# Performance work log

Hardware: AMD Instinct MI355X
Metric: run time of the kernel (lower is better)

## Reference

```python
import jax, jax.numpy as jnp
import numpy as np

MASS = 1.5
DT = 0.01      # physics.refresh_rate
EPS = 1e-6
B, STATE, ACT, T, H = 2048, 12, 4, 128, 512

_NORM = np.zeros(STATE, dtype=np.float32)
_NORM[0] = 4.0 / np.pi; _NORM[1] = 0.5; _NORM[2] = 4.0 / np.pi
_NORM[3] = 0.1; _NORM[4] = 1.0 / 60.0; _NORM[5] = 1.0 / 60.0
_NORM = jnp.asarray(_NORM)  # indices 6:12 stay zero (predict only normalizes 0:6)


def _leaky(x):
    return jnp.where(x >= 0, x, 0.01 * x)


def _mlp(x, W0, b0, W1, b1, W2, b2, W3, b3):
    # 3 hidden LeakyReLU layers + linear head (dropout is eval-mode identity)
    h = _leaky(x @ W0 + b0)
    h = _leaky(h @ W1 + b1)
    h = _leaky(h @ W2 + b2)
    return h @ W3 + b3


def _L_EB(phi, theta, psi):
    cph, sph = jnp.cos(phi), jnp.sin(phi)
    cth, sth = jnp.cos(theta), jnp.sin(theta)
    cps, sps = jnp.cos(psi), jnp.sin(psi)
    r1 = jnp.stack([cth * cps, sph * sth * cps - cph * sps, cph * sth * cps + sph * sps], -1)
    r2 = jnp.stack([cth * sps, sph * sth * sps + cph * cps, cph * sth * sps - sph * cps], -1)
    r3 = jnp.stack([-sth, sph * cth, cph * cth], -1)
    return jnp.stack([r1, r2, r3], -2)  # [B,3,3]


def _derivs(x, forces, I_mat, I_inv):
    V = x[:, 3:6]
    phi, theta = x[:, 6], x[:, 7]
    psi = x[:, 8]
    omega = x[:, 9:12]
    Fv, M = forces[:, 0:3], forces[:, 3:6]
    dpos = jnp.einsum('bij,bj->bi', _L_EB(phi, theta, psi), V)
    dvel = Fv / MASS - jnp.cross(omega, V)
    tth = jnp.tan(theta)
    cth = jnp.clip(jnp.cos(theta), EPS)
    sph, cph = jnp.sin(phi), jnp.cos(phi)
    one, zero = jnp.ones_like(phi), jnp.zeros_like(phi)
    J = jnp.stack([
        jnp.stack([one, sph * tth, cph * tth], -1),
        jnp.stack([zero, cph, -sph], -1),
        jnp.stack([zero, sph / cth, cph / cth], -1)], -2)  # [B,3,3]
    datt = jnp.einsum('bij,bj->bi', J, omega)
    Iw = omega @ I_mat.T                       # I @ omega
    coriolis = jnp.cross(omega, Iw)
    domega = (M - coriolis) @ I_inv.T
    return jnp.concatenate([dpos, dvel, datt, domega], axis=1)


def _rk4(x, forces, I_mat, I_inv):
    f = lambda s: _derivs(s, forces, I_mat, I_inv)
    k1 = f(x)
    k2 = f(x + 0.5 * DT * k1)
    k3 = f(x + 0.5 * DT * k2)
    k4 = f(x + DT * k3)
    return x + (DT / 6.0) * (k1 + 2 * k2 + 2 * k3 + k4)


def _predict(x, act, W, I_mat, I_inv):
    norm_x = x * _NORM
    norm_act = (act - 1500.0) / 500.0
    fn = _mlp(jnp.concatenate([norm_x, norm_act], axis=1), *W)
    zeros = jnp.zeros_like(fn[:, 0])
    forces = jnp.stack([fn[:, 0] - 0.5,
                        fn[:, 1] * -0.4 - 10.0,
                        fn[:, 2] * 0.2 - 0.1,
                        zeros, zeros, zeros], axis=1)
    return forces, _rk4(x, forces, I_mat, I_inv)


def setup_inputs() -> dict:
    key = jax.random.key(0)
    ks = jax.random.split(key, 12)
    x_t = jax.random.normal(ks[0], (B, STATE), dtype=jnp.float32) * 0.1
    act_inps = jax.random.uniform(ks[1], (B, ACT, T), dtype=jnp.float32,
                                  minval=1000.0, maxval=2000.0)
    I_mat = jnp.asarray([[0.02, 0.001, 0.002],
                         [0.001, 0.03, 0.001],
                         [0.002, 0.001, 0.04]], dtype=jnp.float32)
    def lin(k, fi, fo):
        s = np.sqrt(2.0 / (fi + fo)).astype(np.float32)
        return jax.random.normal(k, (fi, fo), dtype=jnp.float32) * s
    dims = [(STATE + ACT, H), (H, H), (H, H), (H, 6)]
    W = {}
    for i, (fi, fo) in enumerate(dims):
        W[f'W{i}'] = lin(ks[2 + i], fi, fo)
        W[f'b{i}'] = jnp.zeros((fo,), dtype=jnp.float32)
    return dict(x_t=x_t, act_inps=act_inps, I_mat=I_mat, seq_len=T, **W)


def reference(x_t, act_inps, I_mat, W0, b0, W1, b1, W2, b2, W3, b3, seq_len):
    I_inv = jnp.linalg.inv(I_mat)
    W = (W0, b0, W1, b1, W2, b2, W3, b3)
    acts = jnp.transpose(act_inps[:, :, 1:seq_len], (2, 0, 1))  # [T-1,B,ACT]

    def step(x, act):
        forces, nx = _predict(x, act, W, I_mat, I_inv)
        return nx, (forces, nx)

    _, (forces_seq, x_seq) = jax.lax.scan(step, x_t, acts)
    stacked = jnp.concatenate([x_t[:, :, None], jnp.transpose(x_seq, (1, 2, 0))], axis=2)  # [B,12,T]
    stackedForces = jnp.transpose(forces_seq, (1, 2, 0))  # [B,6,T-1]
    return stackedForces, stacked
```

## Files before the change

### kernel.cpp

```cpp
#include <hip/hip_runtime.h>
#include <stdint.h>

typedef unsigned short u16;
typedef unsigned int   u32;
typedef __attribute__((ext_vector_type(8))) short short8;
typedef __attribute__((ext_vector_type(4))) float f32x4;

#define B_TOT   2048
#define HID     512
#define T_FULL  128
#define ROWS    32
#define NWG     (B_TOT / ROWS)
#define THREADS 512
#define NT      4

#define W0F_SZ  16384
#define W1F_SZ  262144
#define W3F_SZ  8192
#define WF_TOTAL (W0F_SZ + 2*W1F_SZ + W3F_SZ)

__device__ __forceinline__ u16 f2bf(float f){
  u32 u = __float_as_uint(f);
  u32 r = (u + 0x7FFFu + ((u >> 16) & 1u)) >> 16;
  return (u16)r;
}

__device__ __forceinline__ int lds_idx(int m, int k){
  int chunk = k >> 3;
  return m * 512 + ((chunk ^ (m & 7)) << 3) + (k & 7);
}

__global__ void wm_repack(const float* __restrict__ W0, const float* __restrict__ W1,
                          const float* __restrict__ W2, const float* __restrict__ W3,
                          u16* __restrict__ wf)
{
  int idx = blockIdx.x * blockDim.x + threadIdx.x;
  if (idx >= WF_TOTAL) return;
  int e = idx;
  if (e < W0F_SZ){
    int j = e & 7, l = (e >> 3) & 63, nt = e >> 9;
    int k = ((l >> 4) << 3) + j, n = (nt << 4) + (l & 15);
    wf[idx] = (k < 16) ? f2bf(W0[k * HID + n]) : (u16)0;
    return;
  }
  e -= W0F_SZ;
  if (e < W1F_SZ){
    int j = e & 7, l = (e >> 3) & 63, rest = e >> 9, kt = rest & 15, nt = rest >> 4;
    int k = (kt << 5) + ((l >> 4) << 3) + j, n = (nt << 4) + (l & 15);
    wf[idx] = f2bf(W1[k * HID + n]);
    return;
  }
  e -= W1F_SZ;
  if (e < W1F_SZ){
    int j = e & 7, l = (e >> 3) & 63, rest = e >> 9, kt = rest & 15, nt = rest >> 4;
    int k = (kt << 5) + ((l >> 4) << 3) + j, n = (nt << 4) + (l & 15);
    wf[idx] = f2bf(W2[k * HID + n]);
    return;
  }
  e -= W1F_SZ;
  {
    int j = e & 7, l = (e >> 3) & 63, kt = e >> 9;
    int k = (kt << 5) + ((l >> 4) << 3) + j, n = l & 15;
    wf[idx] = (n < 6) ? f2bf(W3[k * 6 + n]) : (u16)0;
  }
}

__device__ __forceinline__ void invert3(const float* a, float* inv){
  float d = a[0]*(a[4]*a[8]-a[5]*a[7]) - a[1]*(a[3]*a[8]-a[5]*a[6]) + a[2]*(a[3]*a[7]-a[4]*a[6]);
  float id = 1.0f / d;
  inv[0]=(a[4]*a[8]-a[5]*a[7])*id; inv[1]=(a[2]*a[7]-a[1]*a[8])*id; inv[2]=(a[1]*a[5]-a[2]*a[4])*id;
  inv[3]=(a[5]*a[6]-a[3]*a[8])*id; inv[4]=(a[0]*a[8]-a[2]*a[6])*id; inv[5]=(a[2]*a[3]-a[0]*a[5])*id;
  inv[6]=(a[3]*a[7]-a[4]*a[6])*id; inv[7]=(a[1]*a[6]-a[0]*a[7])*id; inv[8]=(a[0]*a[4]-a[1]*a[3])*id;
}

__device__ __forceinline__ void derivs(const float* x, const float* Fv,
                                       const float* I9, const float* Ii, float* dx)
{
  float V0=x[3], V1=x[4], V2=x[5];
  float phi=x[6], th=x[7], psi=x[8];
  float w0=x[9], w1=x[10], w2=x[11];
  float sph=__sinf(phi), cph=__cosf(phi);
  float sth=__sinf(th),  cth=__cosf(th);
  float sps=__sinf(psi), cps=__cosf(psi);
  float r00=cth*cps, r01=sph*sth*cps - cph*sps, r02=cph*sth*cps + sph*sps;
  float r10=cth*sps, r11=sph*sth*sps + cph*cps, r12=cph*sth*sps - sph*cps;
  float r20=-sth,    r21=sph*cth,               r22=cph*cth;
  dx[0]=r00*V0+r01*V1+r02*V2;
  dx[1]=r10*V0+r11*V1+r12*V2;
  dx[2]=r20*V0+r21*V1+r22*V2;
  const float invm = 1.0f/1.5f;
  dx[3]=Fv[0]*invm - (w1*V2 - w2*V1);
  dx[4]=Fv[1]*invm - (w2*V0 - w0*V2);
  dx[5]=Fv[2]*invm - (w0*V1 - w1*V0);
  float tth = sth / cth;
  float rc  = 1.0f / fmaxf(cth, 1e-6f);
  dx[6]= w0 + sph*tth*w1 + cph*tth*w2;
  dx[7]=      cph*w1     - sph*w2;
  dx[8]=      sph*rc*w1  + cph*rc*w2;
  float Iw0=I9[0]*w0+I9[1]*w1+I9[2]*w2;
  float Iw1=I9[3]*w0+I9[4]*w1+I9[5]*w2;
  float Iw2=I9[6]*w0+I9[7]*w1+I9[8]*w2;
  float c0=w1*Iw2-w2*Iw1, c1=w2*Iw0-w0*Iw2, c2=w0*Iw1-w1*Iw0;
  dx[9] = -(Ii[0]*c0+Ii[1]*c1+Ii[2]*c2);
  dx[10]= -(Ii[3]*c0+Ii[4]*c1+Ii[5]*c2);
  dx[11]= -(Ii[6]*c0+Ii[7]*c1+Ii[8]*c2);
}

__device__ __forceinline__ void rk4(float* X, const float* Fv, const float* I9, const float* Ii){
  float k1[12],k2[12],k3[12],k4[12],xt[12];
  derivs(X,Fv,I9,Ii,k1);
  #pragma unroll
  for (int c=0;c<12;++c) xt[c]=X[c]+0.005f*k1[c];
  derivs(xt,Fv,I9,Ii,k2);
  #pragma unroll
  for (int c=0;c<12;++c) xt[c]=X[c]+0.005f*k2[c];
  derivs(xt,Fv,I9,Ii,k3);
  #pragma unroll
  for (int c=0;c<12;++c) xt[c]=X[c]+0.01f*k3[c];
  derivs(xt,Fv,I9,Ii,k4);
  #pragma unroll
  for (int c=0;c<12;++c) X[c]+=(0.01f/6.0f)*(k1[c]+2.0f*k2[c]+2.0f*k3[c]+k4[c]);
}

__device__ __forceinline__ void build_input(u16* bufA, const float* X,
                                            const float* __restrict__ act,
                                            int b, int r, int t)
{
  float vin[16];
  vin[0]=X[0]*1.2732395447351628f;
  vin[1]=X[1]*0.5f;
  vin[2]=X[2]*1.2732395447351628f;
  vin[3]=X[3]*0.1f;
  vin[4]=X[4]*0.016666666666666666f;
  vin[5]=X[5]*0.016666666666666666f;
  #pragma unroll
  for (int c=6;c<12;++c) vin[c]=0.0f;
  #pragma unroll
  for (int a=0;a<4;++a)
    vin[12+a] = (act[(size_t)(b*4+a)*T_FULL + t] - 1500.0f) * 0.002f;
  #pragma unroll
  for (int p=0;p<16;++p){
    u32 pack = 0u;
    if (p < 8) pack = (u32)f2bf(vin[2*p]) | ((u32)f2bf(vin[2*p+1]) << 16);
    ((u32*)bufA)[lds_idx(r, 2*p) >> 1] = pack;
  }
}

template<int KT>
__device__ __forceinline__ void do_layer(const u16* __restrict__ bufIn,
                                         const u16* __restrict__ wfrag,
                                         const float* __restrict__ bias,
                                         u16* __restrict__ bufOut,
                                         int lane, int ntb)
{
  const int lm = lane & 15, half = lane >> 4;
  const int m0 = lm, m1 = 16 + lm;
  const int sw0 = m0 & 7, sw1 = m1 & 7;
  f32x4 acc0[NT], acc1[NT];
  #pragma unroll
  for (int i=0;i<NT;++i){ acc0[i]=(f32x4)0.0f; acc1[i]=(f32x4)0.0f; }

  const u16* wbase = wfrag + (((size_t)ntb*KT*64 + lane) << 3);

  short8 Bf[2][NT];
  short8 A0[2], A1[2];
  {
    const int cb = half;
    A0[0] = *(const short8*)(bufIn + m0*512 + ((cb ^ sw0) << 3));
    A1[0] = *(const short8*)(bufIn + m1*512 + ((cb ^ sw1) << 3));
    #pragma unroll
    for (int i=0;i<NT;++i)
      Bf[0][i] = *(const short8*)(wbase + ((size_t)(i*KT) << 9));
  }
  #pragma unroll
  for (int kt=0; kt<KT; ++kt){
    const int cur = kt & 1, nxt = cur ^ 1;
    if (kt + 1 < KT){
      const int cb = ((kt+1) << 2) + half;
      A0[nxt] = *(const short8*)(bufIn + m0*512 + ((cb ^ sw0) << 3));
      A1[nxt] = *(const short8*)(bufIn + m1*512 + ((cb ^ sw1) << 3));
      #pragma unroll
      for (int i=0;i<NT;++i)
        Bf[nxt][i] = *(const short8*)(wbase + ((size_t)(i*KT + kt + 1) << 9));
    }
    #pragma unroll
    for (int i=0;i<NT;++i){
      acc0[i] = __builtin_amdgcn_mfma_f32_16x16x32_bf16(A0[cur], Bf[cur][i], acc0[i], 0, 0, 0);
      acc1[i] = __builtin_amdgcn_mfma_f32_16x16x32_bf16(A1[cur], Bf[cur][i], acc1[i], 0, 0, 0);
    }
  }
  #pragma unroll
  for (int i=0;i<NT;++i){
    int n = ((ntb + i) << 4) + lm;
    float bv = bias[n];
    #pragma unroll
    for (int reg=0; reg<4; ++reg){
      int r0 = (half << 2) + reg, r1 = 16 + r0;
      float v0 = acc0[i][reg] + bv; v0 = (v0 >= 0.0f) ? v0 : 0.01f*v0;
      float v1 = acc1[i][reg] + bv; v1 = (v1 >= 0.0f) ? v1 : 0.01f*v1;
      bufOut[lds_idx(r0, n)] = f2bf(v0);
      bufOut[lds_idx(r1, n)] = f2bf(v1);
    }
  }
}

__global__ __launch_bounds__(THREADS, 2)
void wm_main(const float* __restrict__ x_t, const float* __restrict__ act,
             const float* __restrict__ Imat, const int* __restrict__ seqlen_p,
             const float* __restrict__ b0, const float* __restrict__ b1,
             const float* __restrict__ b2, const float* __restrict__ b3,
             const u16* __restrict__ wf, float* __restrict__ out)
{
  __shared__ u16 bufA[16384];
  __shared__ u16 bufB[16384];
  float* fscr = (float*)(bufA + 256);
  const int tid  = threadIdx.x;
  const int lane = tid & 63;
  const int wave = tid >> 6;
  const int ntb  = wave * NT;
  const int rowbase = blockIdx.x * ROWS;
  const int steps = seqlen_p[0] - 1;
  const int seqlen = steps + 1;

  const u16* w0f = wf;
  const u16* w1f = wf + W0F_SZ;
  const u16* w2f = w1f + W1F_SZ;
  const u16* w3f = w2f + W1F_SZ;

  float* outF = out;
  float* outX = out + (size_t)B_TOT * 6 * steps;

  float X[12], I9[9], Ii[9];
  if (tid < ROWS){
    const int b = rowbase + tid;
    #pragma unroll
    for (int c=0;c<12;++c){
      float raw = x_t[b*12 + c];
      X[c] = raw;
      outX[(size_t)(b*12 + c)*seqlen] = raw;
    }
    #pragma unroll
    for (int i=0;i<9;++i) I9[i] = Imat[i];
    invert3(I9, Ii);
    build_input(bufA, X, act, b, tid, 1);
  }

  for (int s=0; s<steps; ++s){
    __syncthreads();
    do_layer<1 >(bufA, w0f, b0, bufB, lane, ntb);
    __syncthreads();
    do_layer<16>(bufB, w1f, b1, bufA, lane, ntb);
    __syncthreads();
    do_layer<16>(bufA, w2f, b2, bufB, lane, ntb);
    __syncthreads();
    if (wave == 0){
      const int lm = lane & 15, half = lane >> 4;
      const int m0 = lm, m1 = 16 + lm;
      const int sw0 = m0 & 7, sw1 = m1 & 7;
      short8 w3r[16];
      #pragma unroll
      for (int kt=0; kt<16; ++kt)
        w3r[kt] = *(const short8*)(w3f + (((size_t)kt*64 + lane) << 3));
      f32x4 a3_0 = (f32x4)0.0f, a3_1 = (f32x4)0.0f;
      #pragma unroll
      for (int kt=0; kt<16; ++kt){
        int cb = (kt << 2) + half;
        short8 x0 = *(const short8*)(bufB + m0*512 + ((cb ^ sw0) << 3));
        short8 x1 = *(const short8*)(bufB + m1*512 + ((cb ^ sw1) << 3));
        a3_0 = __builtin_amdgcn_mfma_f32_16x16x32_bf16(x0, w3r[kt], a3_0, 0, 0, 0);
        a3_1 = __builtin_amdgcn_mfma_f32_16x16x32_bf16(x1, w3r[kt], a3_1, 0, 0, 0);
      }
      const int c = lm;
      float bv = (c < 6) ? b3[c] : 0.0f;
      #pragma unroll
      for (int mt=0; mt<2; ++mt){
        #pragma unroll
        for (int reg=0; reg<4; ++reg){
          int rr = (mt << 4) + (half << 2) + reg;
          float fn = ((mt == 0) ? a3_0[reg] : a3_1[reg]) + bv;
          float f;
          if      (c == 0) f = fn - 0.5f;
          else if (c == 1) f = fn * -0.4f - 10.0f;
          else if (c == 2) f = fn * 0.2f - 0.1f;
          else             f = 0.0f;
          if (c < 6){
            int b = rowbase + rr;
            outF[(size_t)(b*6 + c)*steps + s] = f;
          }
          if (c < 3) fscr[rr*3 + c] = f;
        }
      }
      asm volatile("s_waitcnt lgkmcnt(0)" ::: "memory");
      if (tid < ROWS){
        const int b = rowbase + tid;
        float Fv[3] = { fscr[tid*3], fscr[tid*3+1], fscr[tid*3+2] };
        rk4(X, Fv, I9, Ii);
        #pragma unroll
        for (int cc=0;cc<12;++cc)
          outX[(size_t)(b*12 + cc)*seqlen + (s+1)] = X[cc];
        if (s + 1 < steps) build_input(bufA, X, act, b, tid, s + 2);
      }
    }
  }
}

extern "C" void kernel_launch(void* const* d_in, const int* in_sizes, int n_in,
                              void* d_out, int out_size, void* d_ws, size_t ws_size,
                              hipStream_t stream)
{
  const float* x_t  = (const float*)d_in[0];
  const float* act  = (const float*)d_in[1];
  const float* Imat = (const float*)d_in[2];
  const int*   seqp = (const int*)d_in[3];
  const float* W0   = (const float*)d_in[4];
  const float* b0   = (const float*)d_in[5];
  const float* W1   = (const float*)d_in[6];
  const float* b1   = (const float*)d_in[7];
  const float* W2   = (const float*)d_in[8];
  const float* b2   = (const float*)d_in[9];
  const float* W3   = (const float*)d_in[10];
  const float* b3   = (const float*)d_in[11];
  u16* wfrag = (u16*)d_ws;

  hipLaunchKernelGGL(wm_repack, dim3((WF_TOTAL + 255)/256), dim3(256), 0, stream,
                     W0, W1, W2, W3, wfrag);
  hipLaunchKernelGGL(wm_main, dim3(NWG), dim3(THREADS), 0, stream,
                     x_t, act, Imat, seqp, b0, b1, b2, b3, wfrag, (float*)d_out);
}
```

Measured before the change: 6.109 ms.

## Deepen weight prefetch to 4-k-tile blocks and recompute inertia inverse per step

The hidden-layer GEMM now loads weight fragments in blocks of four k-tiles with double buffering, and batches the LDS activation loads per block, where before it prefetched a single k-tile ahead. The aim is to keep more global weight loads in flight and hide their latency behind the MFMA work. The inertia matrix inverse is no longer kept in registers for the whole kernel; it is reloaded and inverted inside each step, which lowers register pressure at the cost of a little redundant scalar work. The larger Bf buffer (32 short8 values) raises VGPR use and may spill or reduce occupancy.

```diff
diff --git a/kernel.cpp b/kernel.cpp
--- a/kernel.cpp
+++ b/kernel.cpp
@@ -162,31 +162,50 @@
 
   const u16* wbase = wfrag + (((size_t)ntb*KT*64 + lane) << 3);
 
-  short8 Bf[2][NT];
-  short8 A0[2], A1[2];
-  {
-    const int cb = half;
-    A0[0] = *(const short8*)(bufIn + m0*512 + ((cb ^ sw0) << 3));
-    A1[0] = *(const short8*)(bufIn + m1*512 + ((cb ^ sw1) << 3));
+  if constexpr (KT == 1){
+    short8 A0 = *(const short8*)(bufIn + m0*512 + ((half ^ sw0) << 3));
+    short8 A1 = *(const short8*)(bufIn + m1*512 + ((half ^ sw1) << 3));
+    short8 Bf[NT];
     #pragma unroll
     for (int i=0;i<NT;++i)
-      Bf[0][i] = *(const short8*)(wbase + ((size_t)(i*KT) << 9));
-  }
-  #pragma unroll
-  for (int kt=0; kt<KT; ++kt){
-    const int cur = kt & 1, nxt = cur ^ 1;
-    if (kt + 1 < KT){
-      const int cb = ((kt+1) << 2) + half;
-      A0[nxt] = *(const short8*)(bufIn + m0*512 + ((cb ^ sw0) << 3));
-      A1[nxt] = *(const short8*)(bufIn + m1*512 + ((cb ^ sw1) << 3));
+      Bf[i] = *(const short8*)(wbase + ((size_t)i << 9));
+    #pragma unroll
+    for (int i=0;i<NT;++i){
+      acc0[i] = __builtin_amdgcn_mfma_f32_16x16x32_bf16(A0, Bf[i], acc0[i], 0, 0, 0);
+      acc1[i] = __builtin_amdgcn_mfma_f32_16x16x32_bf16(A1, Bf[i], acc1[i], 0, 0, 0);
+    }
+  } else {
+    static_assert(KT == 16, "KT must be 1 or 16");
+    short8 Bf[2][4][NT];
+    #pragma unroll
+    for (int j=0;j<4;++j)
       #pragma unroll
       for (int i=0;i<NT;++i)
-        Bf[nxt][i] = *(const short8*)(wbase + ((size_t)(i*KT + kt + 1) << 9));
-    }
-    #pragma unroll
-    for (int i=0;i<NT;++i){
-      acc0[i] = __builtin_amdgcn_mfma_f32_16x16x32_bf16(A0[cur], Bf[cur][i], acc0[i], 0, 0, 0);
-      acc1[i] = __builtin_amdgcn_mfma_f32_16x16x32_bf16(A1[cur], Bf[cur][i], acc1[i], 0, 0, 0);
+        Bf[0][j][i] = *(const short8*)(wbase + ((size_t)(i*KT + j) << 9));
+    #pragma unroll
+    for (int blk=0; blk<4; ++blk){
+      const int cur = blk & 1, nxt = cur ^ 1;
+      if (blk < 3){
+        #pragma unroll
+        for (int j=0;j<4;++j)
+          #pragma unroll
+          for (int i=0;i<NT;++i)
+            Bf[nxt][j][i] = *(const short8*)(wbase + ((size_t)(i*KT + blk*4 + 4 + j) << 9));
+      }
+      short8 A0[4], A1[4];
+      #pragma unroll
+      for (int j=0;j<4;++j){
+        const int cb = ((blk*4 + j) << 2) + half;
+        A0[j] = *(const short8*)(bufIn + m0*512 + ((cb ^ sw0) << 3));
+        A1[j] = *(const short8*)(bufIn + m1*512 + ((cb ^ sw1) << 3));
+      }
+      #pragma unroll
+      for (int j=0;j<4;++j)
+        #pragma unroll
+        for (int i=0;i<NT;++i){
+          acc0[i] = __builtin_amdgcn_mfma_f32_16x16x32_bf16(A0[j], Bf[cur][j][i], acc0[i], 0, 0, 0);
+          acc1[i] = __builtin_amdgcn_mfma_f32_16x16x32_bf16(A1[j], Bf[cur][j][i], acc1[i], 0, 0, 0);
+        }
     }
   }
   #pragma unroll
@@ -230,7 +249,7 @@
   float* outF = out;
   float* outX = out + (size_t)B_TOT * 6 * steps;
 
-  float X[12], I9[9], Ii[9];
+  float X[12];
   if (tid < ROWS){
     const int b = rowbase + tid;
     #pragma unroll
@@ -239,9 +258,6 @@
       X[c] = raw;
       outX[(size_t)(b*12 + c)*seqlen] = raw;
     }
-    #pragma unroll
-    for (int i=0;i<9;++i) I9[i] = Imat[i];
-    invert3(I9, Ii);
     build_input(bufA, X, act, b, tid, 1);
   }
 
@@ -293,6 +309,10 @@
       asm volatile("s_waitcnt lgkmcnt(0)" ::: "memory");
       if (tid < ROWS){
         const int b = rowbase + tid;
+        float I9[9], Ii[9];
+        #pragma unroll
+        for (int i=0;i<9;++i) I9[i] = Imat[i];
+        invert3(I9, Ii);
         float Fv[3] = { fscr[tid*3], fscr[tid*3+1], fscr[tid*3+2] };
         rk4(X, Fv, I9, Ii);
         #pragma unroll
```

New measurement: 5.598 ms. -8.4%, faster.

## Split hidden layers across four cooperating workgroups with global-memory exchange and flags

Applied to the files above, without the earlier changes.

Each 32-row batch group now runs on four workgroups. Each workgroup computes a quarter of the output columns of the two 512x512 hidden layers, then exchanges its slices with the other three through global memory, using per-layer flag counters and spin-waits. Layer 0 weights and the biases are held in registers, and only the first member writes outputs. This gives four times more parallel work per time step, so more CUs are busy, at the cost of two inter-workgroup synchronisations per step through global memory. It also depends on all 256 workgroups being resident at once to avoid deadlock.

```diff
diff --git a/kernel.cpp b/kernel.cpp
--- a/kernel.cpp
+++ b/kernel.cpp
@@ -10,14 +10,16 @@
 #define HID     512
 #define T_FULL  128
 #define ROWS    32
-#define NWG     (B_TOT / ROWS)
+#define NGRP    64
+#define NWG     256
 #define THREADS 512
-#define NT      4
+#define NMEM    4
 
 #define W0F_SZ  16384
 #define W1F_SZ  262144
 #define W3F_SZ  8192
 #define WF_TOTAL (W0F_SZ + 2*W1F_SZ + W3F_SZ)
+#define NFLAGS  (NGRP * 2 * NMEM)
 
 __device__ __forceinline__ u16 f2bf(float f){
   u32 u = __float_as_uint(f);
@@ -35,7 +37,11 @@
                           u16* __restrict__ wf)
 {
   int idx = blockIdx.x * blockDim.x + threadIdx.x;
-  if (idx >= WF_TOTAL) return;
+  if (idx >= WF_TOTAL){
+    int fi = idx - WF_TOTAL;
+    if (fi < NFLAGS) ((u32*)((char*)wf + WF_TOTAL*2 + 4096))[fi] = 0u;
+    return;
+  }
   int e = idx;
   if (e < W0F_SZ){
     int j = e & 7, l = (e >> 3) & 63, nt = e >> 9;
@@ -146,62 +152,61 @@
   }
 }
 
-template<int KT>
-__device__ __forceinline__ void do_layer(const u16* __restrict__ bufIn,
-                                         const u16* __restrict__ wfrag,
-                                         const float* __restrict__ bias,
+__device__ __forceinline__ void layer_ex(const u16* __restrict__ bufIn,
                                          u16* __restrict__ bufOut,
-                                         int lane, int ntb)
+                                         const u16* __restrict__ wL,
+                                         float bvv,
+                                         u16* __restrict__ xgrp,
+                                         u32* __restrict__ flagGrp,
+                                         u32 tag, int mem,
+                                         int lane, int wave, int tid)
 {
   const int lm = lane & 15, half = lane >> 4;
   const int m0 = lm, m1 = 16 + lm;
   const int sw0 = m0 & 7, sw1 = m1 & 7;
-  f32x4 acc0[NT], acc1[NT];
-  #pragma unroll
-  for (int i=0;i<NT;++i){ acc0[i]=(f32x4)0.0f; acc1[i]=(f32x4)0.0f; }
-
-  const u16* wbase = wfrag + (((size_t)ntb*KT*64 + lane) << 3);
-
-  short8 Bf[2][NT];
-  short8 A0[2], A1[2];
+  const int nt = mem * 8 + wave;
+  f32x4 acc0 = (f32x4)0.0f, acc1 = (f32x4)0.0f;
+  const u16* wb = wL + (((size_t)nt * 16) * 64 + lane) * 8;
+  #pragma unroll
+  for (int kt = 0; kt < 16; ++kt){
+    const int cb = (kt << 2) + half;
+    short8 A0 = *(const short8*)(bufIn + m0*512 + ((cb ^ sw0) << 3));
+    short8 A1 = *(const short8*)(bufIn + m1*512 + ((cb ^ sw1) << 3));
+    short8 Bf = *(const short8*)(wb + ((size_t)kt << 9));
+    acc0 = __builtin_amdgcn_mfma_f32_16x16x32_bf16(A0, Bf, acc0, 0, 0, 0);
+    acc1 = __builtin_amdgcn_mfma_f32_16x16x32_bf16(A1, Bf, acc1, 0, 0, 0);
+  }
+  const int n = (nt << 4) + lm;
+  #pragma unroll
+  for (int reg = 0; reg < 4; ++reg){
+    int r0 = (half << 2) + reg, r1 = 16 + r0;
+    float v0 = acc0[reg] + bvv; v0 = (v0 >= 0.0f) ? v0 : 0.01f*v0;
+    float v1 = acc1[reg] + bvv; v1 = (v1 >= 0.0f) ? v1 : 0.01f*v1;
+    bufOut[lds_idx(r0, n)] = f2bf(v0);
+    bufOut[lds_idx(r1, n)] = f2bf(v1);
+  }
+  __syncthreads();
+  const int row = tid >> 4, c16 = tid & 15;
   {
-    const int cb = half;
-    A0[0] = *(const short8*)(bufIn + m0*512 + ((cb ^ sw0) << 3));
-    A1[0] = *(const short8*)(bufIn + m1*512 + ((cb ^ sw1) << 3));
-    #pragma unroll
-    for (int i=0;i<NT;++i)
-      Bf[0][i] = *(const short8*)(wbase + ((size_t)(i*KT) << 9));
-  }
-  #pragma unroll
-  for (int kt=0; kt<KT; ++kt){
-    const int cur = kt & 1, nxt = cur ^ 1;
-    if (kt + 1 < KT){
-      const int cb = ((kt+1) << 2) + half;
-      A0[nxt] = *(const short8*)(bufIn + m0*512 + ((cb ^ sw0) << 3));
-      A1[nxt] = *(const short8*)(bufIn + m1*512 + ((cb ^ sw1) << 3));
-      #pragma unroll
-      for (int i=0;i<NT;++i)
-        Bf[nxt][i] = *(const short8*)(wbase + ((size_t)(i*KT + kt + 1) << 9));
-    }
-    #pragma unroll
-    for (int i=0;i<NT;++i){
-      acc0[i] = __builtin_amdgcn_mfma_f32_16x16x32_bf16(A0[cur], Bf[cur][i], acc0[i], 0, 0, 0);
-      acc1[i] = __builtin_amdgcn_mfma_f32_16x16x32_bf16(A1[cur], Bf[cur][i], acc1[i], 0, 0, 0);
-    }
-  }
-  #pragma unroll
-  for (int i=0;i<NT;++i){
-    int n = ((ntb + i) << 4) + lm;
-    float bv = bias[n];
-    #pragma unroll
-    for (int reg=0; reg<4; ++reg){
-      int r0 = (half << 2) + reg, r1 = 16 + r0;
-      float v0 = acc0[i][reg] + bv; v0 = (v0 >= 0.0f) ? v0 : 0.01f*v0;
-      float v1 = acc1[i][reg] + bv; v1 = (v1 >= 0.0f) ? v1 : 0.01f*v1;
-      bufOut[lds_idx(r0, n)] = f2bf(v0);
-      bufOut[lds_idx(r1, n)] = f2bf(v1);
-    }
-  }
+    short8 v = *(const short8*)(bufOut + row*512 + (((mem << 4) + c16) << 3));
+    *(short8*)(xgrp + ((size_t)mem << 12) + (size_t)tid * 8) = v;
+  }
+  __threadfence();
+  __syncthreads();
+  if (tid == 0) *(volatile u32*)(flagGrp + mem) = tag;
+  #pragma unroll
+  for (int o = 1; o < 4; ++o){
+    const volatile u32* fp = (const volatile u32*)(flagGrp + ((mem + o) & 3));
+    while (*fp < tag) __builtin_amdgcn_s_sleep(2);
+  }
+  __threadfence();
+  #pragma unroll
+  for (int o = 1; o < 4; ++o){
+    const int mm = (mem + o) & 3;
+    short8 v = *(const short8*)(xgrp + ((size_t)mm << 12) + (size_t)tid * 8);
+    *(short8*)(bufOut + row*512 + (((mm << 4) + c16) << 3)) = v;
+  }
+  __syncthreads();
 }
 
 __global__ __launch_bounds__(THREADS, 2)
@@ -209,16 +214,19 @@
              const float* __restrict__ Imat, const int* __restrict__ seqlen_p,
              const float* __restrict__ b0, const float* __restrict__ b1,
              const float* __restrict__ b2, const float* __restrict__ b3,
-             const u16* __restrict__ wf, float* __restrict__ out)
+             const u16* __restrict__ wf, u32* __restrict__ flags,
+             u16* __restrict__ xbuf, float* __restrict__ out)
 {
   __shared__ u16 bufA[16384];
   __shared__ u16 bufB[16384];
   float* fscr = (float*)(bufA + 256);
+
   const int tid  = threadIdx.x;
   const int lane = tid & 63;
   const int wave = tid >> 6;
-  const int ntb  = wave * NT;
-  const int rowbase = blockIdx.x * ROWS;
+  const int g    = blockIdx.x & 63;
+  const int mem  = blockIdx.x >> 6;
+  const int rowbase = g * ROWS;
   const int steps = seqlen_p[0] - 1;
   const int seqlen = steps + 1;
 
@@ -226,33 +234,72 @@
   const u16* w1f = wf + W0F_SZ;
   const u16* w2f = w1f + W1F_SZ;
   const u16* w3f = w2f + W1F_SZ;
+  u16* xg1 = xbuf + ((size_t)(0*NGRP + g) << 14);
+  u16* xg2 = xbuf + ((size_t)(1*NGRP + g) << 14);
+  u32* fl1 = flags + (g*2 + 0)*4;
+  u32* fl2 = flags + (g*2 + 1)*4;
 
   float* outF = out;
   float* outX = out + (size_t)B_TOT * 6 * steps;
 
-  float X[12], I9[9], Ii[9];
+  const int lm0 = lane & 15;
+  short8 w0r[4];
+  float bvL0[4];
+  #pragma unroll
+  for (int i=0;i<4;++i){
+    w0r[i] = *(const short8*)(w0f + (((size_t)(wave*4 + i)*64 + lane) << 3));
+    bvL0[i] = b0[((wave*4 + i) << 4) + lm0];
+  }
+  const int myNt = mem*8 + wave;
+  float bv1 = b1[(myNt << 4) + lm0];
+  float bv2 = b2[(myNt << 4) + lm0];
+  float bv3 = (lm0 < 6) ? b3[lm0] : 0.0f;
+  float I9[9], Ii[9];
+  #pragma unroll
+  for (int i=0;i<9;++i) I9[i] = Imat[i];
+  invert3(I9, Ii);
+
+  float X[12];
+  #pragma unroll
+  for (int c=0;c<12;++c) X[c] = 0.0f;
   if (tid < ROWS){
     const int b = rowbase + tid;
     #pragma unroll
     for (int c=0;c<12;++c){
       float raw = x_t[b*12 + c];
       X[c] = raw;
-      outX[(size_t)(b*12 + c)*seqlen] = raw;
+      if (mem == 0) outX[(size_t)(b*12 + c)*seqlen] = raw;
     }
-    #pragma unroll
-    for (int i=0;i<9;++i) I9[i] = Imat[i];
-    invert3(I9, Ii);
     build_input(bufA, X, act, b, tid, 1);
   }
 
   for (int s=0; s<steps; ++s){
     __syncthreads();
-    do_layer<1 >(bufA, w0f, b0, bufB, lane, ntb);
+    {
+      const int lm = lane & 15, half = lane >> 4;
+      const int m0 = lm, m1 = 16 + lm;
+      const int sw0 = m0 & 7, sw1 = m1 & 7;
+      short8 A0 = *(const short8*)(bufA + m0*512 + ((half ^ sw0) << 3));
+      short8 A1 = *(const short8*)(bufA + m1*512 + ((half ^ sw1) << 3));
+      #pragma unroll
+      for (int i=0;i<4;++i){
+        f32x4 a0 = (f32x4)0.0f, a1 = (f32x4)0.0f;
+        a0 = __builtin_amdgcn_mfma_f32_16x16x32_bf16(A0, w0r[i], a0, 0, 0, 0);
+        a1 = __builtin_amdgcn_mfma_f32_16x16x32_bf16(A1, w0r[i], a1, 0, 0, 0);
+        int n = ((wave*4 + i) << 4) + lm;
+        #pragma unroll
+        for (int reg=0; reg<4; ++reg){
+          int r0 = (half << 2) + reg, r1 = 16 + r0;
+          float v0 = a0[reg] + bvL0[i]; v0 = (v0 >= 0.0f) ? v0 : 0.01f*v0;
+          float v1 = a1[reg] + bvL0[i]; v1 = (v1 >= 0.0f) ? v1 : 0.01f*v1;
+          bufB[lds_idx(r0, n)] = f2bf(v0);
+          bufB[lds_idx(r1, n)] = f2bf(v1);
+        }
+      }
+    }
     __syncthreads();
-    do_layer<16>(bufB, w1f, b1, bufA, lane, ntb);
-    __syncthreads();
-    do_layer<16>(bufA, w2f, b2, bufB, lane, ntb);
-    __syncthreads();
+    layer_ex(bufB, bufA, w1f, bv1, xg1, fl1, (u32)(s+1), mem, lane, wave, tid);
+    layer_ex(bufA, bufB, w2f, bv2, xg2, fl2, (u32)(s+1), mem, lane, wave, tid);
     if (wave == 0){
       const int lm = lane & 15, half = lane >> 4;
       const int m0 = lm, m1 = 16 + lm;
@@ -271,19 +318,18 @@
         a3_1 = __builtin_amdgcn_mfma_f32_16x16x32_bf16(x1, w3r[kt], a3_1, 0, 0, 0);
       }
       const int c = lm;
-      float bv = (c < 6) ? b3[c] : 0.0f;
       #pragma unroll
       for (int mt=0; mt<2; ++mt){
         #pragma unroll
         for (int reg=0; reg<4; ++reg){
           int rr = (mt << 4) + (half << 2) + reg;
-          float fn = ((mt == 0) ? a3_0[reg] : a3_1[reg]) + bv;
+          float fn = ((mt == 0) ? a3_0[reg] : a3_1[reg]) + bv3;
           float f;
           if      (c == 0) f = fn - 0.5f;
           else if (c == 1) f = fn * -0.4f - 10.0f;
           else if (c == 2) f = fn * 0.2f - 0.1f;
           else             f = 0.0f;
-          if (c < 6){
+          if (c < 6 && mem == 0){
             int b = rowbase + rr;
             outF[(size_t)(b*6 + c)*steps + s] = f;
           }
@@ -295,9 +341,11 @@
         const int b = rowbase + tid;
         float Fv[3] = { fscr[tid*3], fscr[tid*3+1], fscr[tid*3+2] };
         rk4(X, Fv, I9, Ii);
-        #pragma unroll
-        for (int cc=0;cc<12;++cc)
-          outX[(size_t)(b*12 + cc)*seqlen + (s+1)] = X[cc];
+        if (mem == 0){
+          #pragma unroll
+          for (int cc=0;cc<12;++cc)
+            outX[(size_t)(b*12 + cc)*seqlen + (s+1)] = X[cc];
+        }
         if (s + 1 < steps) build_input(bufA, X, act, b, tid, s + 2);
       }
     }
@@ -321,9 +369,12 @@
   const float* W3   = (const float*)d_in[10];
   const float* b3   = (const float*)d_in[11];
   u16* wfrag = (u16*)d_ws;
-
-  hipLaunchKernelGGL(wm_repack, dim3((WF_TOTAL + 255)/256), dim3(256), 0, stream,
+  u32* flags = (u32*)((char*)d_ws + WF_TOTAL*2 + 4096);
+  u16* xbuf  = (u16*)((char*)d_ws + WF_TOTAL*2 + 8192);
+
+  hipLaunchKernelGGL(wm_repack, dim3((WF_TOTAL + NFLAGS + 255)/256), dim3(256), 0, stream,
                      W0, W1, W2, W3, wfrag);
   hipLaunchKernelGGL(wm_main, dim3(NWG), dim3(THREADS), 0, stream,
-                     x_t, act, Imat, seqp, b0, b1, b2, b3, wfrag, (float*)d_out);
-}
+                     x_t, act, Imat, seqp, b0, b1, b2, b3, wfrag, flags, xbuf,
+                     (float*)d_out);
+}
```

Result: slower. 20.08 ms (+228.7%).
